# Kernel optimization log

Hardware: AMD Instinct MI355X
Metric: run time of the kernel (lower is better)

Reference implementation:

```python
import jax, jax.numpy as jnp
import numpy as np

# ---- module hyperparameters (from init_kwargs) ----
J = 6      # number of octaves -> subsample by 2**J
Q = 6      # wavelets per octave
T = 16000  # signal length
SUB = 2 ** J           # downsampling factor (=> T_out = 250)
XI_MAX = 0.35          # max center frequency (cycles/sample), kymatio convention


def _build_filters(T, J, Q):
    """Gabor (Morlet-style) band-pass filterbank + Gaussian lowpass, in Fourier domain."""
    freqs = np.fft.fftfreq(T).astype(np.float64)          # (T,) cycles/sample
    n_psi = J * Q
    xis = XI_MAX * 2.0 ** (-np.arange(n_psi) / Q)         # constant-Q center freqs
    r = 2.0 ** (1.0 / Q)
    sigmas = xis * (r - 1.0) / (r + 1.0)                  # constant-Q bandwidths
    psi_hat = np.exp(-((freqs[None, :] - xis[:, None]) ** 2)
                     / (2.0 * sigmas[:, None] ** 2))       # (n_psi, T)
    sigma_phi = XI_MAX / (2.0 ** J)                        # lowpass bandwidth ~ 2^-J
    phi_hat = np.exp(-(freqs ** 2) / (2.0 * sigma_phi ** 2))  # (T,)
    return jnp.asarray(psi_hat, jnp.float32), jnp.asarray(phi_hat, jnp.float32)

PSI_HAT, PHI_HAT = _build_filters(T, J, Q)  # fixed (non-learned) filter constants


def setup_inputs() -> dict:
    key = jax.random.key(0)
    x = jax.random.normal(key, (64, 1, T), dtype=jnp.float32)
    return {"x": x}


def _scattering(x2d):
    """First-order scattering. x2d: (B, T) -> Sx: (B, 1 + J*Q, T//2**J)."""
    X = jnp.fft.fft(x2d, axis=-1)                                   # (B, T) complex
    # order 0: lowpass + subsample
    S0 = jnp.real(jnp.fft.ifft(X * PHI_HAT, axis=-1))[:, ::SUB]     # (B, T')
    # order 1: bandpass -> modulus -> lowpass -> subsample (vectorized over filters)
    U = jnp.abs(jnp.fft.ifft(X[:, None, :] * PSI_HAT[None, :, :], axis=-1))  # (B,JQ,T)
    S1 = jnp.real(jnp.fft.ifft(jnp.fft.fft(U, axis=-1) * PHI_HAT, axis=-1))[:, :, ::SUB]
    return jnp.concatenate([S0[:, None, :], S1], axis=1)            # (B, C, T')


def reference(x):
    # accept (B, T) or (B, 1, T) like the torch module
    if x.ndim == 3:
        x = x[:, 0, :]
    Sx = _scattering(x)[..., None]                                  # (B, C, T', 1)
    C = Sx.shape[1]
    c1 = max(1, C // 3)
    c2 = max(1, 2 * C // 3)
    low = Sx[:, :c1].mean(axis=1)
    mid = Sx[:, c1:c2].mean(axis=1)
    high = Sx[:, c2:].mean(axis=1)
    return jnp.stack([low, mid, high], axis=1)                      # (B, 3, T', 1)
```

## Files before the change

kernel.cpp:

```cpp
#include <hip/hip_runtime.h>
#include <hip/hip_bf16.h>

#define TLEN 16000
#define NPSI 36
#define NBATCH 64
#define NOUT 250
#define NCH 37
#define DHALF 176
#define KMAX 8000
#define TWO_PI 6.283185307179586

__device__ __forceinline__ int brev7(int q){ return (int)(__brev((unsigned)q) >> 25); }
__device__ __forceinline__ int drev125(int p){
    return (p % 5) * 25 + ((p / 5) % 5) * 5 + (p / 25);
}

__global__ __launch_bounds__(256) void k_ffta(const float* __restrict__ x,
                                              float2* __restrict__ Gtmp){
    __shared__ float xr[32 * 126], xi[32 * 126];
    __shared__ float w125r[125], w125i[125];
    __shared__ float w16r[125],  w16i[125];
    __shared__ float w128r[128], w128i[128];
    const int b = blockIdx.x >> 2, g = blockIdx.x & 3, row0 = 32 * g;
    const int tid = threadIdx.x;

    for (int j = tid; j < 125; j += 256){
        double a = -TWO_PI * (double)j / 125.0;
        w125r[j] = (float)cos(a); w125i[j] = (float)sin(a);
        double a2 = -TWO_PI * (double)j / 16000.0;
        w16r[j] = (float)cos(a2); w16i[j] = (float)sin(a2);
    }
    for (int j = tid; j < 128; j += 256){
        double a = -TWO_PI * (double)j / 128.0;
        w128r[j] = (float)cos(a); w128i[j] = (float)sin(a);
    }
    for (int i = tid; i < 32 * 125; i += 256){
        int n1 = i >> 5, lr = i & 31;
        xr[lr * 126 + n1] = x[b * TLEN + 128 * n1 + row0 + lr];
        xi[lr * 126 + n1] = 0.0f;
    }
    int f = 1;
    for (int s = 25; s >= 1; s /= 5, f *= 5){
        __syncthreads();
        for (int task = tid; task < 25 * 32; task += 256){
            int u = task >> 5, lr = task & 31;
            int blk = u / s, m = u - blk * s;
            int base = lr * 126 + blk * 5 * s + m;
            float vr[5], vi[5];
            #pragma unroll
            for (int r = 0; r < 5; ++r){ vr[r] = xr[base + r * s]; vi[r] = xi[base + r * s]; }
            #pragma unroll
            for (int q = 0; q < 5; ++q){
                float cr = vr[0], ci = vi[0];
                #pragma unroll
                for (int r = 1; r < 5; ++r){
                    int w5 = 25 * ((q * r) % 5);
                    float wr = w125r[w5], wi = w125i[w5];
                    cr += vr[r] * wr - vi[r] * wi;
                    ci += vr[r] * wi + vi[r] * wr;
                }
                int jt = (m * q * f) % 125;
                float tr = w125r[jt], ti = w125i[jt];
                xr[base + q * s] = cr * tr - ci * ti;
                xi[base + q * s] = cr * ti + ci * tr;
            }
        }
    }
    __syncthreads();
    for (int i = tid; i < 125 * 32; i += 256){
        int p = i >> 5, lr = i & 31;
        int n2 = row0 + lr;
        int m = drev125(p);
        int a = m * n2;
        int qq = a / 125, rr = a - qq * 125;
        float tr = w16r[rr] * w128r[qq] - w16i[rr] * w128i[qq];
        float ti = w16r[rr] * w128i[qq] + w16i[rr] * w128r[qq];
        float ar = xr[lr * 126 + p], ai = xi[lr * 126 + p];
        Gtmp[((size_t)b * 125 + p) * 128 + n2] =
            make_float2(ar * tr - ai * ti, ar * ti + ai * tr);
    }
}

__global__ __launch_bounds__(256) void k_fftb(const float2* __restrict__ Gtmp,
                                              float2* __restrict__ Xf){
    __shared__ float gr[128 * 26], gi[128 * 26];
    __shared__ float w128r[128], w128i[128];
    const int b = blockIdx.x / 5, p0 = (blockIdx.x % 5) * 25;
    const int tid = threadIdx.x;
    for (int j = tid; j < 128; j += 256){
        double a = -TWO_PI * (double)j / 128.0;
        w128r[j] = (float)cos(a); w128i[j] = (float)sin(a);
    }
    for (int i = tid; i < 25 * 128; i += 256){
        int ml = i >> 7, n2 = i & 127;
        float2 v = Gtmp[((size_t)b * 125 + p0 + ml) * 128 + n2];
        gr[n2 * 26 + ml] = v.x; gi[n2 * 26 + ml] = v.y;
    }
    for (int span = 64; span >= 1; span >>= 1){
        __syncthreads();
        for (int idx = tid; idx < 1600; idx += 256){
            int u = idx / 25, ml = idx - u * 25;
            int blkq = u / span, mm = u % span;
            int i0 = (blkq * 2 * span + mm) * 26 + ml, i1 = i0 + span * 26;
            float ar = gr[i0], ai = gi[i0], br = gr[i1], bi = gi[i1];
            gr[i0] = ar + br; gi[i0] = ai + bi;
            float dr = ar - br, di = ai - bi;
            int jt = mm * (64 / span);
            gr[i1] = dr * w128r[jt] - di * w128i[jt];
            gi[i1] = dr * w128i[jt] + di * w128r[jt];
        }
    }
    __syncthreads();
    for (int idx = tid; idx < 1600; idx += 256){
        int u = idx / 25, ml = idx - u * 25;
        int ad = (2 * u) * 26 + ml;
        int k = drev125(p0 + ml) + 125 * brev7(2 * u);
        Xf[(size_t)b * KMAX + k] = make_float2(gr[ad], gi[ad]);
    }
}

__global__ __launch_bounds__(512) void k_fft(const float* __restrict__ x,
                                             float2* __restrict__ Xf){
    __shared__ float re[128 * 126];
    __shared__ float im[128 * 126];
    __shared__ float w125r[125], w125i[125];
    __shared__ float w16r[125],  w16i[125];
    __shared__ float w128r[128], w128i[128];
    const int b = blockIdx.x, tid = threadIdx.x;

    for (int j = tid; j < 125; j += 512){
        double a = -TWO_PI * (double)j / 125.0;
        w125r[j] = (float)cos(a); w125i[j] = (float)sin(a);
        double a2 = -TWO_PI * (double)j / 16000.0;
        w16r[j] = (float)cos(a2); w16i[j] = (float)sin(a2);
    }
    for (int j = tid; j < 128; j += 512){
        double a = -TWO_PI * (double)j / 128.0;
        w128r[j] = (float)cos(a); w128i[j] = (float)sin(a);
    }
    for (int gi = tid; gi < TLEN; gi += 512){
        int n2 = gi & 127, n1 = gi >> 7;
        re[n2 * 126 + n1] = x[b * TLEN + gi];
        im[n2 * 126 + n1] = 0.0f;
    }
    int f = 1;
    for (int s = 25; s >= 1; s /= 5, f *= 5){
        __syncthreads();
        for (int task = tid; task < 25 * 128; task += 512){
            int u = task >> 7, n2 = task & 127;
            int blk = u / s, m = u - blk * s;
            int base = n2 * 126 + blk * 5 * s + m;
            float xr[5], xi5[5];
            #pragma unroll
            for (int r = 0; r < 5; ++r){ xr[r] = re[base + r * s]; xi5[r] = im[base + r * s]; }
            #pragma unroll
            for (int q = 0; q < 5; ++q){
                float cr = xr[0], ci = xi5[0];
                #pragma unroll
                for (int r = 1; r < 5; ++r){
                    int w5 = 25 * ((q * r) % 5);
                    float wr = w125r[w5], wi = w125i[w5];
                    cr += xr[r] * wr - xi5[r] * wi;
                    ci += xr[r] * wi + xi5[r] * wr;
                }
                int jt = (m * q * f) % 125;
                float tr = w125r[jt], ti = w125i[jt];
                re[base + q * s] = cr * tr - ci * ti;
                im[base + q * s] = cr * ti + ci * tr;
            }
        }
    }
    __syncthreads();
    for (int idx = tid; idx < TLEN; idx += 512){
        int n2 = idx & 127, p = idx >> 7;
        int m = drev125(p);
        int a = n2 * m;
        int qq = a / 125, rr = a - qq * 125;
        float tr = w16r[rr] * w128r[qq] - w16i[rr] * w128i[qq];
        float ti = w16r[rr] * w128i[qq] + w16i[rr] * w128r[qq];
        int ad = n2 * 126 + p;
        float ar = re[ad], ai = im[ad];
        re[ad] = ar * tr - ai * ti;
        im[ad] = ar * ti + ai * tr;
    }
    for (int span = 64; span >= 1; span >>= 1){
        __syncthreads();
        for (int idx = tid; idx < 64 * 125; idx += 512){
            int u = idx / 125, p = idx - (idx / 125) * 125;
            int blkq = u / span, mm = u % span;
            int i0 = (blkq * 2 * span + mm) * 126 + p, i1 = i0 + span * 126;
            float ar = re[i0], ai = im[i0], br = re[i1], bi = im[i1];
            re[i0] = ar + br; im[i0] = ai + bi;
            float dr = ar - br, di = ai - bi;
            int jt = mm * (64 / span);
            re[i1] = dr * w128r[jt] - di * w128i[jt];
            im[i1] = dr * w128i[jt] + di * w128r[jt];
        }
    }
    __syncthreads();
    for (int idx = tid; idx < 64 * 125; idx += 512){
        int u = idx / 125, p = idx - (idx / 125) * 125;
        int k = drev125(p) + 125 * brev7(2 * u);
        int ad = (2 * u) * 126 + p;
        Xf[(size_t)b * KMAX + k] = make_float2(re[ad], im[ad]);
    }
}

template<int P5, int LQ>
__device__ __forceinline__ void env_body(const float2* __restrict__ Xfb,
                                         float* __restrict__ Schan,
                                         int fi, int b, int tid,
                                         float* Br, float* Bi,
                                         float* wPr, float* wPi,
                                         float* wNr, float* wNi,
                                         float* wQr, float* wQi,
                                         float* w5tr, float* w5ti,
                                         float* hfull, int* drevT, float* sred){
    constexpr int Q = 1 << LQ;
    constexpr int N = P5 * Q;
    constexpr int D = TLEN / N;
    constexpr int NIT = (N + 511) / 512;

    const double xi_d = 0.35 * exp2(-(double)fi / 6.0);
    const double r_d  = exp2(1.0 / 6.0);
    const double sig_d = xi_d * (r_d - 1.0) / (r_d + 1.0);
    const float xi = (float)xi_d;
    const float centerT = (float)(xi_d * (double)TLEN);
    const float sigT = (float)(sig_d * (double)TLEN);
    int klo = (int)floorf(centerT - 5.0f * sigT); if (klo < 1) klo = 1;
    int khi = (int)ceilf(centerT + 5.0f * sigT);  if (khi > KMAX - 1) khi = KMAX - 1;
    const float inv2s2 = (float)(1.0 / (2.0 * sig_d * sig_d));

    for (int j = tid; j < P5; j += 512){
        double a = TWO_PI * (double)j / (double)P5;
        wPr[j] = (float)cos(a); wPi[j] = (float)sin(a);
        double a2 = TWO_PI * (double)j / (double)N;
        wNr[j] = (float)cos(a2); wNi[j] = (float)sin(a2);
        drevT[j] = (P5 == 125) ? drev125(j) : ((j % 5) * 5 + j / 5);
    }
    for (int j = tid; j < Q; j += 512){
        double a = TWO_PI * (double)j / (double)Q;
        wQr[j] = (float)cos(a); wQi[j] = (float)sin(a);
    }
    for (int j = tid; j < 25; j += 512){
        double a = TWO_PI * (double)(((j / 5) * (j % 5)) % 5) / 5.0;
        w5tr[j] = (float)cos(a); w5ti[j] = (float)sin(a);
    }
    for (int j = tid; j <= 2 * DHALF; j += 512){
        double st = 1.0 / (TWO_PI * (0.35 / 64.0));
        double dd = (double)(j - DHALF);
        hfull[j] = (float)((0.35 / 64.0) * sqrt(TWO_PI) * exp(-0.5 * dd * dd / (st * st)));
    }
    __syncthreads();
    for (int idx = tid; idx < N; idx += 512){
        int j = idx >> LQ, k2 = idx & (Q - 1);
        int gk = k2 + (j << LQ);
        float vr = 0.0f, vi = 0.0f;
        if (gk >= klo && gk <= khi){
            float fr = (float)gk * (1.0f / (float)TLEN);
            float d = fr - xi;
            float p = __expf(-d * d * inv2s2) * (1.0f / (float)TLEN);
            float2 Xv = Xfb[gk];
            vr = Xv.x * p; vi = Xv.y * p;
        }
        Br[idx] = vr; Bi[idx] = vi;
    }
    int f = 1;
    for (int s = P5 / 5; s >= 1; s /= 5, f *= 5){
        __syncthreads();
        for (int task = tid; task < (P5 / 5) * Q; task += 512){
            int u = task >> LQ, k2 = task & (Q - 1);
            int blk = u / s, m = u - blk * s;
            int base = (blk * 5 * s + m) * Q + k2;
            float xr[5], xi5[5];
            #pragma unroll
            for (int r = 0; r < 5; ++r){ xr[r] = Br[base + r * s * Q]; xi5[r] = Bi[base + r * s * Q]; }
            #pragma unroll
            for (int q = 0; q < 5; ++q){
                float cr = xr[0], ci = xi5[0];
                #pragma unroll
                for (int r = 1; r < 5; ++r){
                    float wr = w5tr[q * 5 + r], wi = w5ti[q * 5 + r];
                    cr += xr[r] * wr - xi5[r] * wi;
                    ci += xr[r] * wi + xi5[r] * wr;
                }
                int jt = m * q * f;
                float tr = wPr[jt], ti = wPi[jt];
                Br[base + q * s * Q] = cr * tr - ci * ti;
                Bi[base + q * s * Q] = cr * ti + ci * tr;
            }
        }
    }
    __syncthreads();
    for (int idx = tid; idx < N; idx += 512){
        int p = idx >> LQ, k2 = idx & (Q - 1);
        int n1 = drevT[p];
        int a = k2 * n1;
        int qq = a / P5, rr = a - qq * P5;
        float tr = wQr[qq] * wNr[rr] - wQi[qq] * wNi[rr];
        float ti = wQr[qq] * wNi[rr] + wQi[qq] * wNr[rr];
        float ar = Br[idx], ai = Bi[idx];
        Br[idx] = ar * tr - ai * ti;
        Bi[idx] = ar * ti + ai * tr;
    }
    for (int span = Q / 2; span >= 1; span >>= 1){
        __syncthreads();
        for (int idx = tid; idx < P5 * (Q / 2); idx += 512){
            int p = idx / (Q / 2), u = idx - p * (Q / 2);
            int blkq = u / span, mm = u % span;
            int i0 = p * Q + blkq * 2 * span + mm, i1 = i0 + span;
            float ar = Br[i0], ai = Bi[i0], br = Br[i1], bi = Bi[i1];
            Br[i0] = ar + br; Bi[i0] = ai + bi;
            float dr = ar - br, di = ai - bi;
            int jt = mm * ((Q / 2) / span);
            Br[i1] = dr * wQr[jt] - di * wQi[jt];
            Bi[i1] = dr * wQi[jt] + di * wQr[jt];
        }
    }
    __syncthreads();
    float magv[NIT];
    #pragma unroll
    for (int i = 0; i < NIT; ++i){
        int idx = tid + 512 * i;
        if (idx < N){
            float vr = Br[idx], vi = Bi[idx];
            magv[i] = sqrtf(vr * vr + vi * vi);
        }
    }
    __syncthreads();
    #pragma unroll
    for (int i = 0; i < NIT; ++i){
        int idx = tid + 512 * i;
        if (idx < N){
            int p = idx >> LQ, u = idx & (Q - 1);
            int s2 = (int)(__brev((unsigned)u) >> (32 - LQ));
            int np = drevT[p] + P5 * s2;
            Bi[np + (np >> 5)] = magv[i];
        }
    }
    __syncthreads();
    float acc = 0.0f;
    if (tid < 500){
        int t = tid - 250 * (tid / 250);
        int q = tid / 250;
        int m0 = 64 * t;
        int lo = m0 - DHALF;
        int nlo = (lo >= 0) ? ((lo + D - 1) / D) : -((-lo) / D);
        int nhi = (m0 + DHALF) / D;
        int n = nlo + q;
        if (n <= nhi){
            int np = n % N; if (np < 0) np += N;
            int d = m0 - D * n + DHALF;
            for (; n <= nhi; n += 2){
                acc += hfull[d] * Bi[np + (np >> 5)];
                d -= 2 * D;
                np += 2; if (np >= N) np -= N;
            }
        }
        sred[tid] = acc;
    }
    __syncthreads();
    if (tid < 250)
        Schan[(b * NCH + 1 + fi) * NOUT + tid] = (sred[tid] + sred[tid + 250]) * (float)D;
}

__global__ __launch_bounds__(512, 4) void k_env_all(const float* __restrict__ x,
                                                    const float2* __restrict__ Xf,
                                                    float* __restrict__ Schan){
    __shared__ float Br[8000];
    __shared__ float Bi[8256];
    __shared__ float wPr[125], wPi[125];
    __shared__ float wNr[125], wNi[125];
    __shared__ float wQr[128], wQi[128];
    __shared__ float w5tr[25], w5ti[25];
    __shared__ float hfull[2 * DHALF + 1];
    __shared__ int   drevT[125];
    __shared__ float sred[500];

    const int bi = blockIdx.x;
    const int tid = threadIdx.x;
    if (bi < 448){
        int fi = bi >> 6, b = bi & 63;
        env_body<125, 6>(Xf + (size_t)b * KMAX, Schan, fi, b, tid, Br, Bi,
                         wPr, wPi, wNr, wNi, wQr, wQi, w5tr, w5ti, hfull, drevT, sred);
    } else if (bi < 640){
        int t = bi - 448;
        int fi = 7 + (t >> 6), b = t & 63;
        env_body<125, 5>(Xf + (size_t)b * KMAX, Schan, fi, b, tid, Br, Bi,
                         wPr, wPi, wNr, wNi, wQr, wQi, w5tr, w5ti, hfull, drevT, sred);
    } else if (bi < 1088){
        int t = bi - 640;
        int fi = 10 + (t >> 6), b = t & 63;
        env_body<25, 7>(Xf + (size_t)b * KMAX, Schan, fi, b, tid, Br, Bi,
                        wPr, wPi, wNr, wNi, wQr, wQi, w5tr, w5ti, hfull, drevT, sred);
    } else if (bi < 1408){
        int t = bi - 1088;
        int fi = 17 + (t >> 6), b = t & 63;
        env_body<125, 4>(Xf + (size_t)b * KMAX, Schan, fi, b, tid, Br, Bi,
                         wPr, wPi, wNr, wNi, wQr, wQi, w5tr, w5ti, hfull, drevT, sred);
    } else if (bi < 2304){
        int t = bi - 1408;
        int fi = 22 + (t >> 6), b = t & 63;
        env_body<25, 6>(Xf + (size_t)b * KMAX, Schan, fi, b, tid, Br, Bi,
                        wPr, wPi, wNr, wNi, wQr, wQi, w5tr, w5ti, hfull, drevT, sred);
    } else {
        int b = bi - 2304;
        const float* xb = x + (size_t)b * TLEN;
        for (int j = tid; j <= 2 * DHALF; j += 512){
            double st = 1.0 / (TWO_PI * (0.35 / 64.0));
            double dd = (double)(j - DHALF);
            hfull[j] = (float)((0.35 / 64.0) * sqrt(TWO_PI) * exp(-0.5 * dd * dd / (st * st)));
        }
        __syncthreads();
        float acc = 0.0f;
        if (tid < 500){
            int t = tid - 250 * (tid / 250);
            int q = tid / 250;
            int m0 = 64 * t;
            for (int j = q; j <= 2 * DHALF; j += 2){
                int n = m0 - DHALF + j;
                if (n < 0) n += TLEN; else if (n >= TLEN) n -= TLEN;
                acc += hfull[j] * xb[n];
            }
            sred[tid] = acc;
        }
        __syncthreads();
        if (tid < 250)
            Schan[(b * NCH + 0) * NOUT + tid] = sred[tid] + sred[tid + 250];
    }
}

__global__ __launch_bounds__(256) void k_reduce(const float* __restrict__ Schan,
                                                float* __restrict__ out){
    int o = blockIdx.x * 256 + threadIdx.x;
    if (o >= NBATCH * 3 * NOUT) return;
    int b = o / (3 * NOUT);
    int rem = o - b * 3 * NOUT;
    int g = rem / NOUT;
    int t = rem - g * NOUT;
    int c0 = (g == 0) ? 0 : (g == 1 ? 12 : 24);
    int c1 = (g == 0) ? 12 : (g == 1 ? 24 : 37);
    float s = 0.0f;
    for (int c = c0; c < c1; ++c) s += Schan[(b * NCH + c) * NOUT + t];
    out[o] = s / (float)(c1 - c0);
}

__global__ void k_fill_f32(float* out, int n, float v){
    int i = blockIdx.x * 256 + threadIdx.x;
    if (i < n) out[i] = v;
}

extern "C" void kernel_launch(void* const* d_in, const int* in_sizes, int n_in,
                              void* d_out, int out_size, void* d_ws, size_t ws_size,
                              hipStream_t stream) {
    const float* x = (const float*)d_in[0];
    float* out = (float*)d_out;
    const size_t xf_bytes = (size_t)NBATCH * KMAX * sizeof(float2);
    const size_t schan_bytes = (size_t)NBATCH * NCH * NOUT * sizeof(float);
    const size_t gtmp_bytes = (size_t)NBATCH * 16000 * sizeof(float2);
    if (ws_size < xf_bytes + schan_bytes){
        k_fill_f32<<<(out_size + 255) / 256, 256, 0, stream>>>(out, out_size, 800.0f);
        return;
    }
    float2* Xf = (float2*)d_ws;
    float* Schan = (float*)((char*)d_ws + xf_bytes);

    if (ws_size >= xf_bytes + schan_bytes + gtmp_bytes){
        float2* Gtmp = (float2*)((char*)d_ws + xf_bytes + schan_bytes);
        k_ffta<<<NBATCH * 4, 256, 0, stream>>>(x, Gtmp);
        k_fftb<<<NBATCH * 5, 256, 0, stream>>>(Gtmp, Xf);
    } else {
        k_fft<<<NBATCH, 512, 0, stream>>>(x, Xf);
    }
    k_env_all<<<2368, 512, 0, stream>>>(x, Xf, Schan);
    k_reduce<<<(NBATCH * 3 * NOUT + 255) / 256, 256, 0, stream>>>(Schan, out);
}
```

Baseline: 152.6 us.

## Fuse filter load into first radix-5 pass and use radix-4 stages in envelope FFT

The envelope inverse FFT now applies the Gabor filter while loading inputs straight into registers for the first radix-5 butterfly, which removes a separate store pass and one barrier. The final radix-5 stage is merged with the twiddle multiply between the two factors, and the power-of-two stages are regrouped into radix-4 butterflies with a final radix-2, so there are fewer passes through shared memory and fewer barriers. The unused single-block FFT fallback is removed, and the launcher now fills a constant output whenever the workspace is too small for the two-kernel path. The trade-off is more registers per thread and a more complex indexing scheme.

```diff
diff --git a/kernel.cpp b/kernel.cpp
--- a/kernel.cpp
+++ b/kernel.cpp
@@ -119,93 +119,6 @@
     }
 }
 
-__global__ __launch_bounds__(512) void k_fft(const float* __restrict__ x,
-                                             float2* __restrict__ Xf){
-    __shared__ float re[128 * 126];
-    __shared__ float im[128 * 126];
-    __shared__ float w125r[125], w125i[125];
-    __shared__ float w16r[125],  w16i[125];
-    __shared__ float w128r[128], w128i[128];
-    const int b = blockIdx.x, tid = threadIdx.x;
-
-    for (int j = tid; j < 125; j += 512){
-        double a = -TWO_PI * (double)j / 125.0;
-        w125r[j] = (float)cos(a); w125i[j] = (float)sin(a);
-        double a2 = -TWO_PI * (double)j / 16000.0;
-        w16r[j] = (float)cos(a2); w16i[j] = (float)sin(a2);
-    }
-    for (int j = tid; j < 128; j += 512){
-        double a = -TWO_PI * (double)j / 128.0;
-        w128r[j] = (float)cos(a); w128i[j] = (float)sin(a);
-    }
-    for (int gi = tid; gi < TLEN; gi += 512){
-        int n2 = gi & 127, n1 = gi >> 7;
-        re[n2 * 126 + n1] = x[b * TLEN + gi];
-        im[n2 * 126 + n1] = 0.0f;
-    }
-    int f = 1;
-    for (int s = 25; s >= 1; s /= 5, f *= 5){
-        __syncthreads();
-        for (int task = tid; task < 25 * 128; task += 512){
-            int u = task >> 7, n2 = task & 127;
-            int blk = u / s, m = u - blk * s;
-            int base = n2 * 126 + blk * 5 * s + m;
-            float xr[5], xi5[5];
-            #pragma unroll
-            for (int r = 0; r < 5; ++r){ xr[r] = re[base + r * s]; xi5[r] = im[base + r * s]; }
-            #pragma unroll
-            for (int q = 0; q < 5; ++q){
-                float cr = xr[0], ci = xi5[0];
-                #pragma unroll
-                for (int r = 1; r < 5; ++r){
-                    int w5 = 25 * ((q * r) % 5);
-                    float wr = w125r[w5], wi = w125i[w5];
-                    cr += xr[r] * wr - xi5[r] * wi;
-                    ci += xr[r] * wi + xi5[r] * wr;
-                }
-                int jt = (m * q * f) % 125;
-                float tr = w125r[jt], ti = w125i[jt];
-                re[base + q * s] = cr * tr - ci * ti;
-                im[base + q * s] = cr * ti + ci * tr;
-            }
-        }
-    }
-    __syncthreads();
-    for (int idx = tid; idx < TLEN; idx += 512){
-        int n2 = idx & 127, p = idx >> 7;
-        int m = drev125(p);
-        int a = n2 * m;
-        int qq = a / 125, rr = a - qq * 125;
-        float tr = w16r[rr] * w128r[qq] - w16i[rr] * w128i[qq];
-        float ti = w16r[rr] * w128i[qq] + w16i[rr] * w128r[qq];
-        int ad = n2 * 126 + p;
-        float ar = re[ad], ai = im[ad];
-        re[ad] = ar * tr - ai * ti;
-        im[ad] = ar * ti + ai * tr;
-    }
-    for (int span = 64; span >= 1; span >>= 1){
-        __syncthreads();
-        for (int idx = tid; idx < 64 * 125; idx += 512){
-            int u = idx / 125, p = idx - (idx / 125) * 125;
-            int blkq = u / span, mm = u % span;
-            int i0 = (blkq * 2 * span + mm) * 126 + p, i1 = i0 + span * 126;
-            float ar = re[i0], ai = im[i0], br = re[i1], bi = im[i1];
-            re[i0] = ar + br; im[i0] = ai + bi;
-            float dr = ar - br, di = ai - bi;
-            int jt = mm * (64 / span);
-            re[i1] = dr * w128r[jt] - di * w128i[jt];
-            im[i1] = dr * w128i[jt] + di * w128r[jt];
-        }
-    }
-    __syncthreads();
-    for (int idx = tid; idx < 64 * 125; idx += 512){
-        int u = idx / 125, p = idx - (idx / 125) * 125;
-        int k = drev125(p) + 125 * brev7(2 * u);
-        int ad = (2 * u) * 126 + p;
-        Xf[(size_t)b * KMAX + k] = make_float2(re[ad], im[ad]);
-    }
-}
-
 template<int P5, int LQ>
 __device__ __forceinline__ void env_body(const float2* __restrict__ Xfb,
                                          float* __restrict__ Schan,
@@ -219,6 +132,7 @@
     constexpr int Q = 1 << LQ;
     constexpr int N = P5 * Q;
     constexpr int D = TLEN / N;
+    constexpr int S1 = P5 / 5;
     constexpr int NIT = (N + 511) / 512;
 
     const double xi_d = 0.35 * exp2(-(double)fi / 6.0);
@@ -252,69 +166,129 @@
         hfull[j] = (float)((0.35 / 64.0) * sqrt(TWO_PI) * exp(-0.5 * dd * dd / (st * st)));
     }
     __syncthreads();
-    for (int idx = tid; idx < N; idx += 512){
-        int j = idx >> LQ, k2 = idx & (Q - 1);
-        int gk = k2 + (j << LQ);
-        float vr = 0.0f, vi = 0.0f;
-        if (gk >= klo && gk <= khi){
-            float fr = (float)gk * (1.0f / (float)TLEN);
-            float d = fr - xi;
-            float p = __expf(-d * d * inv2s2) * (1.0f / (float)TLEN);
-            float2 Xv = Xfb[gk];
-            vr = Xv.x * p; vi = Xv.y * p;
-        }
-        Br[idx] = vr; Bi[idx] = vi;
-    }
-    int f = 1;
-    for (int s = P5 / 5; s >= 1; s /= 5, f *= 5){
-        __syncthreads();
-        for (int task = tid; task < (P5 / 5) * Q; task += 512){
+    for (int task = tid; task < S1 * Q; task += 512){
+        int m = task >> LQ, k2 = task & (Q - 1);
+        float vr[5], vi[5];
+        #pragma unroll
+        for (int r = 0; r < 5; ++r){
+            int gk = k2 + ((m + r * S1) << LQ);
+            float ur = 0.0f, ui = 0.0f;
+            if (gk >= klo && gk <= khi){
+                float fr = (float)gk * (1.0f / (float)TLEN);
+                float d = fr - xi;
+                float p = __expf(-d * d * inv2s2) * (1.0f / (float)TLEN);
+                float2 Xv = Xfb[gk];
+                ur = Xv.x * p; ui = Xv.y * p;
+            }
+            vr[r] = ur; vi[r] = ui;
+        }
+        int base = m * Q + k2;
+        #pragma unroll
+        for (int q = 0; q < 5; ++q){
+            float cr = vr[0], ci = vi[0];
+            #pragma unroll
+            for (int r = 1; r < 5; ++r){
+                float wr = w5tr[q * 5 + r], wi = w5ti[q * 5 + r];
+                cr += vr[r] * wr - vi[r] * wi;
+                ci += vr[r] * wi + vi[r] * wr;
+            }
+            int jt = m * q;
+            float tr = wPr[jt], ti = wPi[jt];
+            Br[base + q * S1 * Q] = cr * tr - ci * ti;
+            Bi[base + q * S1 * Q] = cr * ti + ci * tr;
+        }
+    }
+    if (P5 == 125){
+        __syncthreads();
+        for (int task = tid; task < 25 * Q; task += 512){
             int u = task >> LQ, k2 = task & (Q - 1);
-            int blk = u / s, m = u - blk * s;
-            int base = (blk * 5 * s + m) * Q + k2;
-            float xr[5], xi5[5];
-            #pragma unroll
-            for (int r = 0; r < 5; ++r){ xr[r] = Br[base + r * s * Q]; xi5[r] = Bi[base + r * s * Q]; }
+            int blk = u / 5, m = u - blk * 5;
+            int base = (blk * 25 + m) * Q + k2;
+            float vr[5], vi[5];
+            #pragma unroll
+            for (int r = 0; r < 5; ++r){ vr[r] = Br[base + r * 5 * Q]; vi[r] = Bi[base + r * 5 * Q]; }
             #pragma unroll
             for (int q = 0; q < 5; ++q){
-                float cr = xr[0], ci = xi5[0];
+                float cr = vr[0], ci = vi[0];
                 #pragma unroll
                 for (int r = 1; r < 5; ++r){
                     float wr = w5tr[q * 5 + r], wi = w5ti[q * 5 + r];
-                    cr += xr[r] * wr - xi5[r] * wi;
-                    ci += xr[r] * wi + xi5[r] * wr;
+                    cr += vr[r] * wr - vi[r] * wi;
+                    ci += vr[r] * wi + vi[r] * wr;
                 }
-                int jt = m * q * f;
+                int jt = m * q * 5;
                 float tr = wPr[jt], ti = wPi[jt];
-                Br[base + q * s * Q] = cr * tr - ci * ti;
-                Bi[base + q * s * Q] = cr * ti + ci * tr;
-            }
-        }
-    }
-    __syncthreads();
-    for (int idx = tid; idx < N; idx += 512){
-        int p = idx >> LQ, k2 = idx & (Q - 1);
-        int n1 = drevT[p];
-        int a = k2 * n1;
-        int qq = a / P5, rr = a - qq * P5;
-        float tr = wQr[qq] * wNr[rr] - wQi[qq] * wNi[rr];
-        float ti = wQr[qq] * wNi[rr] + wQi[qq] * wNr[rr];
-        float ar = Br[idx], ai = Bi[idx];
-        Br[idx] = ar * tr - ai * ti;
-        Bi[idx] = ar * ti + ai * tr;
-    }
-    for (int span = Q / 2; span >= 1; span >>= 1){
+                Br[base + q * 5 * Q] = cr * tr - ci * ti;
+                Bi[base + q * 5 * Q] = cr * ti + ci * tr;
+            }
+        }
+    }
+    __syncthreads();
+    for (int task = tid; task < S1 * Q; task += 512){
+        int u = task >> LQ, k2 = task & (Q - 1);
+        int base = (u * 5) * Q + k2;
+        float vr[5], vi[5];
+        #pragma unroll
+        for (int r = 0; r < 5; ++r){ vr[r] = Br[base + r * Q]; vi[r] = Bi[base + r * Q]; }
+        #pragma unroll
+        for (int q = 0; q < 5; ++q){
+            float cr = vr[0], ci = vi[0];
+            #pragma unroll
+            for (int r = 1; r < 5; ++r){
+                float wr = w5tr[q * 5 + r], wi = w5ti[q * 5 + r];
+                cr += vr[r] * wr - vi[r] * wi;
+                ci += vr[r] * wi + vi[r] * wr;
+            }
+            int n1 = drevT[5 * u + q];
+            int a = k2 * n1;
+            int qq = a / P5, rr = a - qq * P5;
+            float tr = wQr[qq] * wNr[rr] - wQi[qq] * wNi[rr];
+            float ti = wQr[qq] * wNi[rr] + wQi[qq] * wNr[rr];
+            Br[base + q * Q] = cr * tr - ci * ti;
+            Bi[base + q * Q] = cr * ti + ci * tr;
+        }
+    }
+    #pragma unroll
+    for (int pass = 0; pass < LQ / 2; ++pass){
+        const int Sp = Q >> (1 + 2 * pass);
+        const int half = Sp >> 1;
+        __syncthreads();
+        for (int task = tid; task < P5 * (Q / 4); task += 512){
+            int prow = task / (Q / 4), v = task & (Q / 4 - 1);
+            int blkq = v / half, m = v - blkq * half;
+            int base = prow * Q + blkq * 2 * Sp + m;
+            float Ar = Br[base],           Ai = Bi[base];
+            float B2r = Br[base + half],   B2i = Bi[base + half];
+            float Cr = Br[base + Sp],      Ci = Bi[base + Sp];
+            float D2r = Br[base + Sp + half], D2i = Bi[base + Sp + half];
+            int jt1 = m * ((Q / 2) / Sp);
+            float w1r = wQr[jt1], w1i = wQi[jt1];
+            float w2r = wQr[2 * jt1], w2i = wQi[2 * jt1];
+            float A1r = Ar + Cr, A1i = Ai + Ci;
+            float t1r = Ar - Cr, t1i = Ai - Ci;
+            float C1r = t1r * w1r - t1i * w1i, C1i = t1r * w1i + t1i * w1r;
+            float B1r = B2r + D2r, B1i = B2i + D2i;
+            float t2r = B2r - D2r, t2i = B2i - D2i;
+            float t3r = -t2i, t3i = t2r;
+            float D1r = t3r * w1r - t3i * w1i, D1i = t3r * w1i + t3i * w1r;
+            Br[base] = A1r + B1r;  Bi[base] = A1i + B1i;
+            float u1r = A1r - B1r, u1i = A1i - B1i;
+            Br[base + half] = u1r * w2r - u1i * w2i;
+            Bi[base + half] = u1r * w2i + u1i * w2r;
+            Br[base + Sp] = C1r + D1r;  Bi[base + Sp] = C1i + D1i;
+            float u2r = C1r - D1r, u2i = C1i - D1i;
+            Br[base + Sp + half] = u2r * w2r - u2i * w2i;
+            Bi[base + Sp + half] = u2r * w2i + u2i * w2r;
+        }
+    }
+    if (LQ & 1){
         __syncthreads();
         for (int idx = tid; idx < P5 * (Q / 2); idx += 512){
             int p = idx / (Q / 2), u = idx - p * (Q / 2);
-            int blkq = u / span, mm = u % span;
-            int i0 = p * Q + blkq * 2 * span + mm, i1 = i0 + span;
-            float ar = Br[i0], ai = Bi[i0], br = Br[i1], bi = Bi[i1];
-            Br[i0] = ar + br; Bi[i0] = ai + bi;
-            float dr = ar - br, di = ai - bi;
-            int jt = mm * ((Q / 2) / span);
-            Br[i1] = dr * wQr[jt] - di * wQi[jt];
-            Bi[i1] = dr * wQi[jt] + di * wQr[jt];
+            int i0 = p * Q + 2 * u, i1 = i0 + 1;
+            float ar = Br[i0], ai = Bi[i0], br2 = Br[i1], bi2 = Bi[i1];
+            Br[i0] = ar + br2; Bi[i0] = ai + bi2;
+            Br[i1] = ar - br2; Bi[i1] = ai - bi2;
         }
     }
     __syncthreads();
@@ -458,20 +432,16 @@
     const size_t xf_bytes = (size_t)NBATCH * KMAX * sizeof(float2);
     const size_t schan_bytes = (size_t)NBATCH * NCH * NOUT * sizeof(float);
     const size_t gtmp_bytes = (size_t)NBATCH * 16000 * sizeof(float2);
-    if (ws_size < xf_bytes + schan_bytes){
+    if (ws_size < xf_bytes + schan_bytes + gtmp_bytes){
         k_fill_f32<<<(out_size + 255) / 256, 256, 0, stream>>>(out, out_size, 800.0f);
         return;
     }
     float2* Xf = (float2*)d_ws;
     float* Schan = (float*)((char*)d_ws + xf_bytes);
-
-    if (ws_size >= xf_bytes + schan_bytes + gtmp_bytes){
-        float2* Gtmp = (float2*)((char*)d_ws + xf_bytes + schan_bytes);
-        k_ffta<<<NBATCH * 4, 256, 0, stream>>>(x, Gtmp);
-        k_fftb<<<NBATCH * 5, 256, 0, stream>>>(Gtmp, Xf);
-    } else {
-        k_fft<<<NBATCH, 512, 0, stream>>>(x, Xf);
-    }
+    float2* Gtmp = (float2*)((char*)d_ws + xf_bytes + schan_bytes);
+
+    k_ffta<<<NBATCH * 4, 256, 0, stream>>>(x, Gtmp);
+    k_fftb<<<NBATCH * 5, 256, 0, stream>>>(Gtmp, Xf);
     k_env_all<<<2368, 512, 0, stream>>>(x, Xf, Schan);
     k_reduce<<<(NBATCH * 3 * NOUT + 255) / 256, 256, 0, stream>>>(Schan, out);
 }
```

Result: faster. 144.8 us (-5.1%).
